# Kernel tuning notes

Hardware: AMD Instinct MI355X
Metric: run time of the kernel (lower is better)

Reference implementation:

```python
import jax, jax.numpy as jnp
import numpy as np

T, B, D, H = 2048, 32, 256, 256


def setup_inputs() -> dict:
    key = jax.random.key(0)
    ks = jax.random.split(key, 7)
    s = 1.0 / np.sqrt(H)
    return {
        "seq_embs": jax.random.normal(ks[0], (T, B, D), dtype=jnp.float32),
        "mask_x": jax.random.randint(ks[1], (T, B), 0, 2, dtype=jnp.int32),
        "hidden": jax.random.normal(ks[2], (B, H), dtype=jnp.float32),
        "w_ih": jax.random.uniform(ks[3], (3 * H, D), jnp.float32, -s, s),
        "w_hh": jax.random.uniform(ks[4], (3 * H, H), jnp.float32, -s, s),
        "b_ih": jax.random.uniform(ks[5], (3 * H,), jnp.float32, -s, s),
        "b_hh": jax.random.uniform(ks[6], (3 * H,), jnp.float32, -s, s),
    }


def reference(seq_embs, mask_x, hidden, w_ih, w_hh, b_ih, b_hh):
    # Precompute all input-side gate projections in one big GEMM: [T, B, 3H]
    gi_all = jnp.einsum("tbd,gd->tbg", seq_embs, w_ih) + b_ih
    mask_f = mask_x.astype(seq_embs.dtype)  # [T, B]

    def step(h, inp):
        gi, m_t = inp  # gi: [B, 3H], m_t: [B]
        gh = h @ w_hh.T + b_hh  # [B, 3H]
        i_r, i_z, i_n = jnp.split(gi, 3, axis=1)
        h_r, h_z, h_n = jnp.split(gh, 3, axis=1)
        r = jax.nn.sigmoid(i_r + h_r)
        z = jax.nn.sigmoid(i_z + h_z)
        n = jnp.tanh(i_n + r * h_n)
        h_t = (1.0 - z) * n + z * h  # GRUCell candidate hidden
        m = m_t[:, None]  # [B, 1]
        h_new = h_t * m + h * (1.0 - m)  # mask-gated state update
        return h_new, h_t * m  # output per step is masked candidate

    h_final, outputs = jax.lax.scan(step, hidden, (gi_all, mask_f))
    return outputs, h_final
```

## Files before the change

kernel.cpp:

```cpp
#include <hip/hip_runtime.h>
#include <hip/hip_bf16.h>

#define TT 2048
#define BB 32
#define DD 256
#define HH 256
#define GG 768

typedef _Float16 half2_t __attribute__((ext_vector_type(2)));

__device__ inline float fdot2(unsigned int w, unsigned int h, float acc) {
#if __has_builtin(__builtin_amdgcn_fdot2)
    return __builtin_amdgcn_fdot2(__builtin_bit_cast(half2_t, w),
                                  __builtin_bit_cast(half2_t, h), acc, false);
#else
    half2_t a = __builtin_bit_cast(half2_t, w);
    half2_t b = __builtin_bit_cast(half2_t, h);
    return acc + (float)a.x * (float)b.x + (float)a.y * (float)b.y;
#endif
}

__device__ inline void store4(float* p, float a, float b, float c, float d) {
    *(float4*)p = make_float4(a, b, c, d);
}
__device__ inline void store4(__hip_bfloat16* p, float a, float b, float c, float d) {
    p[0] = __float2bfloat16(a);
    p[1] = __float2bfloat16(b);
    p[2] = __float2bfloat16(c);
    p[3] = __float2bfloat16(d);
}
__device__ inline float ldgi(const float* p) { return *p; }
__device__ inline float ldgi(const __hip_bfloat16* p) { return __bfloat162float(*p); }

__global__ __launch_bounds__(256)
void pack_w(const float* __restrict__ w, unsigned int* __restrict__ wpk) {
    int i = blockIdx.x * 256 + threadIdx.x;
    int q = i / GG;
    int j = i - q * GG;
    float a = w[(size_t)j * DD + 2 * q];
    float b = w[(size_t)j * DD + 2 * q + 1];
    half2_t h = {(_Float16)a, (_Float16)b};
    wpk[i] = __builtin_bit_cast(unsigned int, h);
}

template <typename GiT>
__global__ __launch_bounds__(256)
void gemm_gi(const float* __restrict__ A,
             const float* __restrict__ W,
             const float* __restrict__ bias,
             GiT* __restrict__ C)
{
    __shared__ float As[32][68];
    __shared__ float Ws[32][68];
    const int tid = threadIdx.x;
    const int bm = blockIdx.y * 64;
    const int bn = blockIdx.x * 64;
    const int tm = (tid & 15) * 4;
    const int tn = (tid >> 4) * 4;
    const int r  = tid >> 3;
    const int c4 = (tid & 7) * 4;

    float acc[4][4] = {};

    for (int k0 = 0; k0 < 256; k0 += 32) {
#pragma unroll
        for (int rr = 0; rr < 64; rr += 32) {
            float4 a = *(const float4*)&A[(size_t)(bm + r + rr) * 256 + k0 + c4];
            As[c4 + 0][r + rr] = a.x;
            As[c4 + 1][r + rr] = a.y;
            As[c4 + 2][r + rr] = a.z;
            As[c4 + 3][r + rr] = a.w;
            float4 w = *(const float4*)&W[(size_t)(bn + r + rr) * 256 + k0 + c4];
            Ws[c4 + 0][r + rr] = w.x;
            Ws[c4 + 1][r + rr] = w.y;
            Ws[c4 + 2][r + rr] = w.z;
            Ws[c4 + 3][r + rr] = w.w;
        }
        __syncthreads();
#pragma unroll
        for (int kk = 0; kk < 32; ++kk) {
            float4 a = *(const float4*)&As[kk][tm];
            float4 w = *(const float4*)&Ws[kk][tn];
            float av[4] = {a.x, a.y, a.z, a.w};
            float wv[4] = {w.x, w.y, w.z, w.w};
#pragma unroll
            for (int i = 0; i < 4; ++i)
#pragma unroll
                for (int j = 0; j < 4; ++j)
                    acc[i][j] += av[i] * wv[j];
        }
        __syncthreads();
    }
#pragma unroll
    for (int i = 0; i < 4; ++i) {
        GiT* cp = C + (size_t)(bm + tm + i) * GG + bn + tn;
        store4(cp, acc[i][0] + bias[bn + tn + 0],
                   acc[i][1] + bias[bn + tn + 1],
                   acc[i][2] + bias[bn + tn + 2],
                   acc[i][3] + bias[bn + tn + 3]);
    }
}

template <typename GiT>
__global__ __launch_bounds__(768, 3)
void gru_scan(const GiT* __restrict__ gi,
              const int* __restrict__ mask,
              const float* __restrict__ h0,
              const unsigned int* __restrict__ wpk,
              const float* __restrict__ b_hh,
              float* __restrict__ out,
              float* __restrict__ hfin)
{
    const int b = blockIdx.x;
    const int j = threadIdx.x;
    __shared__ __align__(16) _Float16 hhalf[HH];
    __shared__ float gh_lds[GG];
    __shared__ int mlds[TT];

    unsigned int w[128];
#pragma unroll
    for (int q = 0; q < 128; ++q)
        w[q] = wpk[q * GG + j];
#pragma unroll
    for (int q = 0; q < 128; ++q)
        asm volatile("" : "+v"(w[q]));

    for (int t = j; t < TT; t += GG)
        mlds[t] = mask[t * BB + b];

    float h_r = 0.f;
    if (j < HH) {
        h_r = h0[b * HH + j];
        hhalf[j] = (_Float16)h_r;
    }
    const float bhh = b_hh[j];
    __syncthreads();

    const uint4* hu4 = (const uint4*)hhalf;

    for (int t = 0; t < TT; ++t) {
        if (mlds[t]) {
            float ir = 0.f, iz = 0.f, inn = 0.f;
            if (j < HH) {
                const GiT* gtb = gi + ((size_t)t * BB + b) * GG;
                ir  = ldgi(gtb + j);
                iz  = ldgi(gtb + j + HH);
                inn = ldgi(gtb + j + 2 * HH);
            }

            float a0 = bhh, a1 = 0.f, a2 = 0.f, a3 = 0.f;
#pragma unroll
            for (int q4 = 0; q4 < 32; ++q4) {
                uint4 hv = hu4[q4];
                a0 = fdot2(w[4 * q4 + 0], hv.x, a0);
                a1 = fdot2(w[4 * q4 + 1], hv.y, a1);
                a2 = fdot2(w[4 * q4 + 2], hv.z, a2);
                a3 = fdot2(w[4 * q4 + 3], hv.w, a3);
            }
            gh_lds[j] = (a0 + a1) + (a2 + a3);
            __syncthreads();

            if (j < HH) {
                float hr = gh_lds[j];
                float hz = gh_lds[j + HH];
                float hn = gh_lds[j + 2 * HH];
                float r = 1.f / (1.f + __expf(-(ir + hr)));
                float z = 1.f / (1.f + __expf(-(iz + hz)));
                float e = __expf(2.f * (inn + r * hn));
                float n = 1.f - 2.f / (e + 1.f);
                float ht = (1.f - z) * n + z * h_r;
                out[((size_t)t * BB + b) * HH + j] = ht;
                h_r = ht;
                hhalf[j] = (_Float16)ht;
            }
            __syncthreads();
        } else {
            if (j < HH)
                out[((size_t)t * BB + b) * HH + j] = 0.f;
        }
    }
    if (j < HH) hfin[b * HH + j] = h_r;
}

extern "C" void kernel_launch(void* const* d_in, const int* in_sizes, int n_in,
                              void* d_out, int out_size, void* d_ws, size_t ws_size,
                              hipStream_t stream) {
    const float* seq  = (const float*)d_in[0];
    const int*   mask = (const int*)  d_in[1];
    const float* h0   = (const float*)d_in[2];
    const float* w_ih = (const float*)d_in[3];
    const float* w_hh = (const float*)d_in[4];
    const float* b_ih = (const float*)d_in[5];
    const float* b_hh = (const float*)d_in[6];

    float* out  = (float*)d_out;
    float* hfin = out + (size_t)TT * BB * HH;

    const size_t wpk_elems = (size_t)128 * GG;
    unsigned int* wpk = (unsigned int*)d_ws;
    const size_t gi_elems = (size_t)TT * BB * GG;
    const size_t need_f32 = wpk_elems * 4 + gi_elems * 4;

    pack_w<<<(128 * GG) / 256, 256, 0, stream>>>(w_hh, wpk);

    dim3 ggrid(GG / 64, (TT * BB) / 64);
    if (ws_size >= need_f32) {
        float* gip = (float*)d_ws + wpk_elems;
        gemm_gi<float><<<ggrid, 256, 0, stream>>>(seq, w_ih, b_ih, gip);
        gru_scan<float><<<BB, GG, 0, stream>>>(gip, mask, h0, wpk, b_hh, out, hfin);
    } else {
        __hip_bfloat16* gip = (__hip_bfloat16*)((float*)d_ws + wpk_elems);
        gemm_gi<__hip_bfloat16><<<ggrid, 256, 0, stream>>>(seq, w_ih, b_ih, gip);
        gru_scan<__hip_bfloat16><<<BB, GG, 0, stream>>>(gip, mask, h0, wpk, b_hh, out, hfin);
    }
}
```

Measured before the change: 1.772 ms.

## Use 512-thread GRU scan with split columns and uint4 weight layout

Shrinks the recurrent scan block from 768 to 512 threads. The first 512 gate columns get a full 256-K dot product per thread. The last 256 columns are split across thread pairs, each doing half the K range, and the halves are combined with a lane shuffle. The weight packing is rearranged into uint4-interleaved layouts so each thread loads its 96 registers of fp16 weights with vector loads. The bias add moves to the gate stage. This cuts the number of waves per block and the per-step barrier cost, at the cost of an extra shuffle and uneven work between the two thread groups.

Result: slower. 2.035 ms (+14.8%).

```diff
diff --git a/kernel.cpp b/kernel.cpp
--- a/kernel.cpp
+++ b/kernel.cpp
@@ -33,14 +33,23 @@
 __device__ inline float ldgi(const __hip_bfloat16* p) { return __bfloat162float(*p); }
 
 __global__ __launch_bounds__(256)
-void pack_w(const float* __restrict__ w, unsigned int* __restrict__ wpk) {
+void pack_w(const float* __restrict__ w, unsigned int* __restrict__ wf) {
     int i = blockIdx.x * 256 + threadIdx.x;
-    int q = i / GG;
-    int j = i - q * GG;
-    float a = w[(size_t)j * DD + 2 * q];
-    float b = w[(size_t)j * DD + 2 * q + 1];
+    int col, k;
+    if (i < 65536) {
+        int comp = i & 3, t = (i >> 2) & 511, q4 = i >> 11;
+        col = t;
+        k = 8 * q4 + 2 * comp;
+    } else {
+        int i2 = i - 65536;
+        int comp = i2 & 3, t = (i2 >> 2) & 511, p4 = i2 >> 11;
+        col = 512 + (t >> 1);
+        k = (t & 1) * 128 + 8 * p4 + 2 * comp;
+    }
+    float a = w[(size_t)col * DD + k];
+    float b = w[(size_t)col * DD + k + 1];
     half2_t h = {(_Float16)a, (_Float16)b};
-    wpk[i] = __builtin_bit_cast(unsigned int, h);
+    wf[i] = __builtin_bit_cast(unsigned int, h);
 }
 
 template <typename GiT>
@@ -102,7 +111,7 @@
 }
 
 template <typename GiT>
-__global__ __launch_bounds__(768, 3)
+__global__ __launch_bounds__(512, 2)
 void gru_scan(const GiT* __restrict__ gi,
               const int* __restrict__ mask,
               const float* __restrict__ h0,
@@ -112,74 +121,95 @@
               float* __restrict__ hfin)
 {
     const int b = blockIdx.x;
-    const int j = threadIdx.x;
+    const int t = threadIdx.x;
     __shared__ __align__(16) _Float16 hhalf[HH];
     __shared__ float gh_lds[GG];
     __shared__ int mlds[TT];
 
-    unsigned int w[128];
-#pragma unroll
-    for (int q = 0; q < 128; ++q)
-        w[q] = wpk[q * GG + j];
-#pragma unroll
-    for (int q = 0; q < 128; ++q)
-        asm volatile("" : "+v"(w[q]));
-
-    for (int t = j; t < TT; t += GG)
-        mlds[t] = mask[t * BB + b];
-
-    float h_r = 0.f;
-    if (j < HH) {
-        h_r = h0[b * HH + j];
-        hhalf[j] = (_Float16)h_r;
-    }
-    const float bhh = b_hh[j];
+    uint4 wA[32];
+    uint4 wB[16];
+    {
+        const uint4* wp = (const uint4*)wpk;
+#pragma unroll
+        for (int q4 = 0; q4 < 32; ++q4)
+            wA[q4] = wp[q4 * 512 + t];
+        const uint4* wpB = wp + 32 * 512;
+#pragma unroll
+        for (int p4 = 0; p4 < 16; ++p4)
+            wB[p4] = wpB[p4 * 512 + t];
+    }
+
+    for (int i = t; i < TT; i += 512)
+        mlds[i] = mask[i * BB + b];
+
+    float h_r = 0.f, bh0 = 0.f, bh1 = 0.f, bh2 = 0.f;
+    if (t < HH) {
+        h_r = h0[b * HH + t];
+        hhalf[t] = (_Float16)h_r;
+        bh0 = b_hh[t];
+        bh1 = b_hh[t + HH];
+        bh2 = b_hh[t + 2 * HH];
+    }
     __syncthreads();
 
     const uint4* hu4 = (const uint4*)hhalf;
-
-    for (int t = 0; t < TT; ++t) {
-        if (mlds[t]) {
+    const uint4* hB  = (const uint4*)(hhalf + (t & 1) * 128);
+
+    for (int ts = 0; ts < TT; ++ts) {
+        if (mlds[ts]) {
             float ir = 0.f, iz = 0.f, inn = 0.f;
-            if (j < HH) {
-                const GiT* gtb = gi + ((size_t)t * BB + b) * GG;
-                ir  = ldgi(gtb + j);
-                iz  = ldgi(gtb + j + HH);
-                inn = ldgi(gtb + j + 2 * HH);
-            }
-
-            float a0 = bhh, a1 = 0.f, a2 = 0.f, a3 = 0.f;
+            if (t < HH) {
+                const GiT* gtb = gi + ((size_t)ts * BB + b) * GG;
+                ir  = ldgi(gtb + t);
+                iz  = ldgi(gtb + t + HH);
+                inn = ldgi(gtb + t + 2 * HH);
+            }
+
+            float a0 = 0.f, a1 = 0.f, a2 = 0.f, a3 = 0.f;
 #pragma unroll
             for (int q4 = 0; q4 < 32; ++q4) {
                 uint4 hv = hu4[q4];
-                a0 = fdot2(w[4 * q4 + 0], hv.x, a0);
-                a1 = fdot2(w[4 * q4 + 1], hv.y, a1);
-                a2 = fdot2(w[4 * q4 + 2], hv.z, a2);
-                a3 = fdot2(w[4 * q4 + 3], hv.w, a3);
-            }
-            gh_lds[j] = (a0 + a1) + (a2 + a3);
+                a0 = fdot2(wA[q4].x, hv.x, a0);
+                a1 = fdot2(wA[q4].y, hv.y, a1);
+                a2 = fdot2(wA[q4].z, hv.z, a2);
+                a3 = fdot2(wA[q4].w, hv.w, a3);
+            }
+            float c0 = 0.f, c1 = 0.f, c2 = 0.f, c3 = 0.f;
+#pragma unroll
+            for (int p4 = 0; p4 < 16; ++p4) {
+                uint4 hv = hB[p4];
+                c0 = fdot2(wB[p4].x, hv.x, c0);
+                c1 = fdot2(wB[p4].y, hv.y, c1);
+                c2 = fdot2(wB[p4].z, hv.z, c2);
+                c3 = fdot2(wB[p4].w, hv.w, c3);
+            }
+            float accB = (c0 + c1) + (c2 + c3);
+            float accBo = __shfl_xor(accB, 1);
+            gh_lds[t] = (a0 + a1) + (a2 + a3);
+            if (!(t & 1))
+                gh_lds[512 + (t >> 1)] = accB + accBo;
             __syncthreads();
 
-            if (j < HH) {
-                float hr = gh_lds[j];
-                float hz = gh_lds[j + HH];
-                float hn = gh_lds[j + 2 * HH];
+            if (t < HH) {
+                float hr = gh_lds[t] + bh0;
+                float hz = gh_lds[t + HH] + bh1;
+                float hn = gh_lds[t + 2 * HH] + bh2;
                 float r = 1.f / (1.f + __expf(-(ir + hr)));
                 float z = 1.f / (1.f + __expf(-(iz + hz)));
                 float e = __expf(2.f * (inn + r * hn));
                 float n = 1.f - 2.f / (e + 1.f);
                 float ht = (1.f - z) * n + z * h_r;
-                out[((size_t)t * BB + b) * HH + j] = ht;
+                out[((size_t)ts * BB + b) * HH + t] = ht;
                 h_r = ht;
-                hhalf[j] = (_Float16)ht;
+                hhalf[t] = (_Float16)ht;
             }
             __syncthreads();
         } else {
-            if (j < HH)
-                out[((size_t)t * BB + b) * HH + j] = 0.f;
+            if (t < HH)
+                out[((size_t)ts * BB + b) * HH + t] = 0.f;
         }
     }
-    if (j < HH) hfin[b * HH + j] = h_r;
+    if (t < HH) hfin[b * HH + t] = h_r;
 }
 
 extern "C" void kernel_launch(void* const* d_in, const int* in_sizes, int n_in,
@@ -207,10 +237,10 @@
     if (ws_size >= need_f32) {
         float* gip = (float*)d_ws + wpk_elems;
         gemm_gi<float><<<ggrid, 256, 0, stream>>>(seq, w_ih, b_ih, gip);
-        gru_scan<float><<<BB, GG, 0, stream>>>(gip, mask, h0, wpk, b_hh, out, hfin);
+        gru_scan<float><<<BB, 512, 0, stream>>>(gip, mask, h0, wpk, b_hh, out, hfin);
     } else {
         __hip_bfloat16* gip = (__hip_bfloat16*)((float*)d_ws + wpk_elems);
         gemm_gi<__hip_bfloat16><<<ggrid, 256, 0, stream>>>(seq, w_ih, b_ih, gip);
-        gru_scan<__hip_bfloat16><<<BB, GG, 0, stream>>>(gip, mask, h0, wpk, b_hh, out, hfin);
-    }
-}
+        gru_scan<__hip_bfloat16><<<BB, 512, 0, stream>>>(gip, mask, h0, wpk, b_hh, out, hfin);
+    }
+}
```

## Stream recurrent weights from global memory with an 8-deep register ring buffer

Applied to the files above, without the earlier changes.

The scan kernel no longer keeps all 128 packed half2 weights of its column in registers for the whole sequence. It repacks W_hh into uint4-interleaved chunks and streams them from global/L2 each step through an 8-entry register buffer, prefetched ahead of use and refilled before the barrier. This frees a large share of VGPRs, but adds about 24 KB of L2/global weight traffic per step per workgroup on the serial critical path, where load latency may not be hidden.

After: 3.924 ms. +121.5%, slower.

```diff
diff --git a/kernel.cpp b/kernel.cpp
--- a/kernel.cpp
+++ b/kernel.cpp
@@ -33,14 +33,17 @@
 __device__ inline float ldgi(const __hip_bfloat16* p) { return __bfloat162float(*p); }
 
 __global__ __launch_bounds__(256)
-void pack_w(const float* __restrict__ w, unsigned int* __restrict__ wpk) {
+void pack_w(const float* __restrict__ w, unsigned int* __restrict__ wf) {
     int i = blockIdx.x * 256 + threadIdx.x;
-    int q = i / GG;
-    int j = i - q * GG;
-    float a = w[(size_t)j * DD + 2 * q];
-    float b = w[(size_t)j * DD + 2 * q + 1];
+    int c  = i & 3;
+    int e  = i >> 2;
+    int q4 = e / GG;
+    int j  = e - q4 * GG;
+    int k  = q4 * 8 + 2 * c;
+    float a = w[(size_t)j * DD + k];
+    float b = w[(size_t)j * DD + k + 1];
     half2_t h = {(_Float16)a, (_Float16)b};
-    wpk[i] = __builtin_bit_cast(unsigned int, h);
+    wf[i] = __builtin_bit_cast(unsigned int, h);
 }
 
 template <typename GiT>
@@ -106,7 +109,7 @@
 void gru_scan(const GiT* __restrict__ gi,
               const int* __restrict__ mask,
               const float* __restrict__ h0,
-              const unsigned int* __restrict__ wpk,
+              const uint4* __restrict__ wq4,
               const float* __restrict__ b_hh,
               float* __restrict__ out,
               float* __restrict__ hfin)
@@ -117,16 +120,8 @@
     __shared__ float gh_lds[GG];
     __shared__ int mlds[TT];
 
-    unsigned int w[128];
-#pragma unroll
-    for (int q = 0; q < 128; ++q)
-        w[q] = wpk[q * GG + j];
-#pragma unroll
-    for (int q = 0; q < 128; ++q)
-        asm volatile("" : "+v"(w[q]));
-
-    for (int t = j; t < TT; t += GG)
-        mlds[t] = mask[t * BB + b];
+    for (int i = j; i < TT; i += GG)
+        mlds[i] = mask[i * BB + b];
 
     float h_r = 0.f;
     if (j < HH) {
@@ -134,15 +129,23 @@
         hhalf[j] = (_Float16)h_r;
     }
     const float bhh = b_hh[j];
+
+    const uint4* wj = wq4 + j;
+
+    uint4 wbuf[8];
+#pragma unroll
+    for (int q4 = 0; q4 < 8; ++q4)
+        wbuf[q4] = wj[(size_t)q4 * GG];
+
     __syncthreads();
 
     const uint4* hu4 = (const uint4*)hhalf;
 
-    for (int t = 0; t < TT; ++t) {
-        if (mlds[t]) {
+    for (int ts = 0; ts < TT; ++ts) {
+        if (mlds[ts]) {
             float ir = 0.f, iz = 0.f, inn = 0.f;
             if (j < HH) {
-                const GiT* gtb = gi + ((size_t)t * BB + b) * GG;
+                const GiT* gtb = gi + ((size_t)ts * BB + b) * GG;
                 ir  = ldgi(gtb + j);
                 iz  = ldgi(gtb + j + HH);
                 inn = ldgi(gtb + j + 2 * HH);
@@ -152,12 +155,20 @@
 #pragma unroll
             for (int q4 = 0; q4 < 32; ++q4) {
                 uint4 hv = hu4[q4];
-                a0 = fdot2(w[4 * q4 + 0], hv.x, a0);
-                a1 = fdot2(w[4 * q4 + 1], hv.y, a1);
-                a2 = fdot2(w[4 * q4 + 2], hv.z, a2);
-                a3 = fdot2(w[4 * q4 + 3], hv.w, a3);
+                uint4 wv = wbuf[q4 & 7];
+                a0 = fdot2(wv.x, hv.x, a0);
+                a1 = fdot2(wv.y, hv.y, a1);
+                a2 = fdot2(wv.z, hv.z, a2);
+                a3 = fdot2(wv.w, hv.w, a3);
+                if (q4 + 8 < 32)
+                    wbuf[q4 & 7] = wj[(size_t)(q4 + 8) * GG];
             }
             gh_lds[j] = (a0 + a1) + (a2 + a3);
+
+#pragma unroll
+            for (int q4 = 0; q4 < 8; ++q4)
+                wbuf[q4] = wj[(size_t)q4 * GG];
+
             __syncthreads();
 
             if (j < HH) {
@@ -169,14 +180,14 @@
                 float e = __expf(2.f * (inn + r * hn));
                 float n = 1.f - 2.f / (e + 1.f);
                 float ht = (1.f - z) * n + z * h_r;
-                out[((size_t)t * BB + b) * HH + j] = ht;
+                out[((size_t)ts * BB + b) * HH + j] = ht;
                 h_r = ht;
                 hhalf[j] = (_Float16)ht;
             }
             __syncthreads();
         } else {
             if (j < HH)
-                out[((size_t)t * BB + b) * HH + j] = 0.f;
+                out[((size_t)ts * BB + b) * HH + j] = 0.f;
         }
     }
     if (j < HH) hfin[b * HH + j] = h_r;
@@ -196,21 +207,24 @@
     float* out  = (float*)d_out;
     float* hfin = out + (size_t)TT * BB * HH;
 
-    const size_t wpk_elems = (size_t)128 * GG;
-    unsigned int* wpk = (unsigned int*)d_ws;
+    const size_t w_u32 = (size_t)128 * GG;
+    unsigned int* wf = (unsigned int*)d_ws;
     const size_t gi_elems = (size_t)TT * BB * GG;
-    const size_t need_f32 = wpk_elems * 4 + gi_elems * 4;
-
-    pack_w<<<(128 * GG) / 256, 256, 0, stream>>>(w_hh, wpk);
+    const size_t need_f32 = w_u32 * 4 + gi_elems * 4;
+
+    pack_w<<<(int)(w_u32 / 256), 256, 0, stream>>>(w_hh, wf);
 
     dim3 ggrid(GG / 64, (TT * BB) / 64);
     if (ws_size >= need_f32) {
-        float* gip = (float*)d_ws + wpk_elems;
+        float* gip = (float*)d_ws + w_u32;
         gemm_gi<float><<<ggrid, 256, 0, stream>>>(seq, w_ih, b_ih, gip);
-        gru_scan<float><<<BB, GG, 0, stream>>>(gip, mask, h0, wpk, b_hh, out, hfin);
+        gru_scan<float><<<BB, GG, 0, stream>>>(gip, mask, h0, (const uint4*)wf,
+                                               b_hh, out, hfin);
     } else {
-        __hip_bfloat16* gip = (__hip_bfloat16*)((float*)d_ws + wpk_elems);
+        __hip_bfloat16* gip = (__hip_bfloat16*)((float*)d_ws + w_u32);
         gemm_gi<__hip_bfloat16><<<ggrid, 256, 0, stream>>>(seq, w_ih, b_ih, gip);
-        gru_scan<__hip_bfloat16><<<BB, GG, 0, stream>>>(gip, mask, h0, wpk, b_hh, out, hfin);
-    }
-}
+        gru_scan<__hip_bfloat16><<<BB, GG, 0, stream>>>(gip, mask, h0,
+                                                        (const uint4*)wf,
+                                                        b_hh, out, hfin);
+    }
+}
```
